# Optimization experiments

Hardware: AMD Instinct MI355X
Metric: run time of the kernel (lower is better)

## Reference

```python
import jax, jax.numpy as jnp
import numpy as np

EMBED = 256
HEADS = 8
HDIM = EMBED // HEADS
TGT = 32400      # bs*H*W = 1*180*180 BEV queries
KLEN = 16896     # bs*num_cams*h*w = 1*6*32*88 image-feature keys
EPS = 1e-5
NEG = -1e9


def _mlp(x, w1, b1, w2, b2):
    # Linear(d,2d) -> ReLU -> Linear(2d,d), torch Linear math with [in,out] weights
    return jax.nn.relu(x @ w1 + b1) @ w2 + b2


def setup_inputs() -> dict:
    rng = np.random.default_rng(0)
    lengths = rng.integers(8, 41, size=KLEN)          # ragged interval sizes
    starts = np.concatenate([[0], np.cumsum(lengths)[:-1]]).astype(np.int32)
    N = int(lengths.sum())
    ranks_feat = np.repeat(np.arange(KLEN, dtype=np.int32), lengths)
    ranks_bev = rng.integers(0, TGT, size=N).astype(np.int32)
    ref_num = int(lengths.max())

    key = jax.random.key(0)
    ks = jax.random.split(key, 16)
    def lin(k, fan_in, fan_out):
        return jax.random.normal(k, (fan_in, fan_out), jnp.float32) / np.sqrt(fan_in)
    return {
        "query": jax.random.normal(ks[0], (TGT, EMBED), jnp.float32),
        "key_in": jax.random.normal(ks[1], (KLEN, EMBED), jnp.float32),
        "value": jax.random.normal(ks[2], (KLEN, EMBED), jnp.float32),
        "ranks_feat": jnp.asarray(ranks_feat),
        "ranks_bev": jnp.asarray(ranks_bev),
        "interval_starts": jnp.asarray(starts),
        "interval_lengths": jnp.asarray(lengths.astype(np.int32)),
        "wq1": lin(ks[3], EMBED, 2 * EMBED), "bq1": jnp.zeros((2 * EMBED,), jnp.float32),
        "wq2": lin(ks[4], 2 * EMBED, EMBED), "bq2": jnp.zeros((EMBED,), jnp.float32),
        "wk1": lin(ks[5], EMBED, 2 * EMBED), "bk1": jnp.zeros((2 * EMBED,), jnp.float32),
        "wk2": lin(ks[6], 2 * EMBED, EMBED), "bk2": jnp.zeros((EMBED,), jnp.float32),
        "ln_g": jnp.ones((EMBED,), jnp.float32), "ln_b": jnp.zeros((EMBED,), jnp.float32),
        "ref_num": ref_num,
    }


def reference(query, key_in, value, ranks_feat, ranks_bev, interval_starts,
              interval_lengths, wq1, bq1, wq2, bq2, wk1, bk1, wk2, bk2,
              ln_g, ln_b, ref_num):
    # interval_lengths only fixes ref_num (static); padding handled via NEG fill.
    N = ranks_feat.shape[0]
    scaling = float(HDIM) ** -0.5

    q = _mlp(query, wq1, bq1, wq2, bq2) * scaling          # [TGT, D]
    k = _mlp(key_in, wk1, bk1, wk2, bk2)                   # [KLEN, D]
    q = q.reshape(TGT, HEADS, HDIM)
    k = k.reshape(KLEN, HEADS, HDIM)
    v = value.reshape(KLEN, HEADS, HDIM)

    # slot index j of each point inside its interval (depth position)
    idx = jnp.arange(N, dtype=jnp.int32)
    seg = jnp.searchsorted(interval_starts, idx, side='right') - 1
    j = idx - interval_starts[seg]

    # per-point q.k logits: q gathered by BEV cell, k by image-feature pixel
    logits = jnp.einsum('nhd,nhd->nh', q[ranks_bev], k[ranks_feat])  # [N,H]

    # dense ragged weight tensor [KLEN, HEADS, ref_num], pad = -1e9
    W = jnp.full((KLEN, HEADS, ref_num), NEG, jnp.float32)
    W = W.at[ranks_feat, :, j].set(logits)
    W_sm = jax.nn.softmax(W, axis=-1)                      # softmax over depth slots

    # gather softmaxed weight per point, weight value, scatter-add to BEV cell
    wp = W_sm[ranks_feat, :, j]                            # [N,H]
    contrib = wp[:, :, None] * v[ranks_feat]               # [N,H,HDIM]
    out = jax.ops.segment_sum(contrib, ranks_bev, num_segments=TGT)
    out = out.reshape(TGT, EMBED)

    # dropout is identity in eval; LayerNorm over embed dim
    mu = jnp.mean(out, axis=-1, keepdims=True)
    var = jnp.mean(jnp.square(out - mu), axis=-1, keepdims=True)
    out = (out - mu) * jax.lax.rsqrt(var + EPS) * ln_g + ln_b
    return out, W_sm
```

## Files before the change

### kernel.cpp

```cpp
#include <hip/hip_runtime.h>
#include <math.h>

#define TGT 32400
#define KLEN 16896
#define EMBED 256
#define HID 512
#define HEADS 8
#define LN_EPS 1e-5f

#define NQT 1013
#define NKT 528
#define HROWS ((NQT + NKT) * 32)

typedef __attribute__((ext_vector_type(8))) short bf16x8;
typedef __attribute__((ext_vector_type(4))) short bf16x4;
typedef __attribute__((ext_vector_type(4))) float f32x4;

__device__ inline short f2bf(float f) {
    union { float f; unsigned u; } v; v.f = f;
    unsigned r = v.u + 0x7FFF + ((v.u >> 16) & 1);
    return (short)(r >> 16);
}
__device__ inline float bf2f(short s) {
    union { unsigned u; float f; } v;
    v.u = ((unsigned)(unsigned short)s) << 16;
    return v.f;
}
__device__ inline void gload_lds16(const short* g, short* l) {
    __builtin_amdgcn_global_load_lds(
        (const __attribute__((address_space(1))) void*)g,
        (__attribute__((address_space(3))) void*)l,
        16, 0, 0);
}

__device__ inline float wave_sum(float v) {
#pragma unroll
    for (int o = 32; o; o >>= 1) v += __shfl_xor(v, o);
    return v;
}
__device__ inline int wave_incl_scan(int v) {
    int lane = threadIdx.x & 63;
#pragma unroll
    for (int o = 1; o < 64; o <<= 1) {
        int x = __shfl_up(v, o);
        if (lane >= o) v += x;
    }
    return v;
}

__global__ __launch_bounds__(256) void prep_kernel(
    const float* __restrict__ value, short* __restrict__ v8,
    const float* __restrict__ wq1, const float* __restrict__ wq2,
    const float* __restrict__ wk1, const float* __restrict__ wk2,
    short* __restrict__ Wt,
    const int* __restrict__ rbev, int N, int* __restrict__ count)
{
    int bid = blockIdx.x;
    if (bid < 2112) {
        int idx = bid * 256 + threadIdx.x;
        int f = idx >> 5;
        int ch = idx & 31;
        const float4* s4 = (const float4*)(value + (size_t)f * 256 + ch * 8);
        float4 a = s4[0], b = s4[1];
        bf16x8 pk;
        pk[0] = f2bf(a.x); pk[1] = f2bf(a.y); pk[2] = f2bf(a.z); pk[3] = f2bf(a.w);
        pk[4] = f2bf(b.x); pk[5] = f2bf(b.y); pk[6] = f2bf(b.z); pk[7] = f2bf(b.w);
        int head = ch >> 2;
        int within = (ch & 3) * 8;
        *(bf16x8*)(v8 + ((size_t)head * KLEN + f) * 32 + within) = pk;
    } else if (bid < 4160) {
        int i = (bid - 2112) * 256 + threadIdx.x;
        int m = i >> 17;
        int r17 = i & 131071;
        int logC = (m & 1) ? 8 : 9;
        int C = 1 << logC;
        int c = r17 & (C - 1);
        int r = r17 >> logC;
        int R = 131072 >> logC;
        const float* W = (m == 0) ? wq1 : (m == 1) ? wq2 : (m == 2) ? wk1 : wk2;
        Wt[(size_t)m * 131072 + (size_t)c * R + r] = f2bf(W[r17]);
    } else {
        int n = (bid - 4160) * 256 + threadIdx.x;
        if (n < N) atomicAdd(&count[rbev[n]], 1);
    }
}

#define XPAD 264
__global__ __launch_bounds__(512, 2) void mlpA_kernel(
    const float* __restrict__ Xq, const float* __restrict__ Xk,
    const short* __restrict__ Wt,
    const float* __restrict__ bq1, const float* __restrict__ bk1,
    short* __restrict__ Hg, int nQblocks)
{
    __shared__ short sX[2][32 * XPAD];

    const int t = threadIdx.x;
    const int wid = t >> 6, lane = t & 63;
    const int lrow = lane & 15, kch = lane >> 4;

    const bool isQ = (int)blockIdx.x < nQblocks;
    const int bid = isQ ? blockIdx.x : blockIdx.x - nQblocks;
    const int stride = isQ ? nQblocks : (gridDim.x - nQblocks);
    const int nT = isQ ? NQT : NKT;
    const int M = isQ ? TGT : KLEN;
    const float* X = isQ ? Xq : Xk;
    const short* W1t = Wt + (size_t)(isQ ? 0 : 2) * 131072;
    const float* b1 = isQ ? bq1 : bk1;
    const int hbase = isQ ? 0 : NQT * 32;

    const int colBase = 64 * wid + lrow;

    bf16x8 w1r[8][4];
#pragma unroll
    for (int ks = 0; ks < 8; ++ks)
#pragma unroll
        for (int j = 0; j < 4; ++j)
            w1r[ks][j] = *(const bf16x8*)(W1t + (size_t)(colBase + 16 * j) * 256 + 32 * ks + 8 * kch);
    float4 bb[4];
#pragma unroll
    for (int j = 0; j < 4; ++j)
        bb[j] = *(const float4*)(b1 + 64 * wid + 16 * j + 4 * kch);

    const int srow = t >> 4, sp = t & 15;

    float4 r0[4], r1[4];
    int tile = bid;
    if (tile < nT) {
        int gr = tile * 32 + srow; if (gr > M - 1) gr = M - 1;
        const float* base = X + (size_t)gr * 256;
#pragma unroll
        for (int i = 0; i < 4; ++i) r0[i] = *(const float4*)(base + (sp + 16 * i) * 4);
    }
    int sel = 0;

    for (; tile < nT; tile += stride) {
#pragma unroll
        for (int i = 0; i < 4; ++i) {
            int c = sp + 16 * i;
            bf16x4 pk;
            pk[0] = f2bf(r0[i].x); pk[1] = f2bf(r0[i].y);
            pk[2] = f2bf(r0[i].z); pk[3] = f2bf(r0[i].w);
            *(bf16x4*)&sX[sel][srow * XPAD + c * 4] = pk;
        }
        int nx = tile + stride;
        if (nx < nT) {
            int gr = nx * 32 + srow; if (gr > M - 1) gr = M - 1;
            const float* base = X + (size_t)gr * 256;
#pragma unroll
            for (int i = 0; i < 4; ++i) r1[i] = *(const float4*)(base + (sp + 16 * i) * 4);
        }
        asm volatile("s_waitcnt lgkmcnt(0)" ::: "memory");
        __builtin_amdgcn_sched_barrier(0);
        __builtin_amdgcn_s_barrier();
        asm volatile("" ::: "memory");

        f32x4 acc[2][4];
#pragma unroll
        for (int rt = 0; rt < 2; ++rt)
#pragma unroll
            for (int j = 0; j < 4; ++j) acc[rt][j] = (f32x4){0.f, 0.f, 0.f, 0.f};

        const short* xs = sX[sel];
#pragma unroll
        for (int ks = 0; ks < 8; ++ks) {
            bf16x8 af[2];
#pragma unroll
            for (int rt = 0; rt < 2; ++rt)
                af[rt] = *(const bf16x8*)&xs[(16 * rt + lrow) * XPAD + 32 * ks + 8 * kch];
#pragma unroll
            for (int j = 0; j < 4; ++j)
#pragma unroll
                for (int rt = 0; rt < 2; ++rt)
                    acc[rt][j] = __builtin_amdgcn_mfma_f32_16x16x32_bf16(w1r[ks][j], af[rt], acc[rt][j], 0, 0, 0);
        }

        int hr0 = hbase + tile * 32;
#pragma unroll
        for (int j = 0; j < 4; ++j) {
#pragma unroll
            for (int rt = 0; rt < 2; ++rt) {
                bf16x4 pk;
                pk[0] = f2bf(fmaxf(acc[rt][j][0] + bb[j].x, 0.f));
                pk[1] = f2bf(fmaxf(acc[rt][j][1] + bb[j].y, 0.f));
                pk[2] = f2bf(fmaxf(acc[rt][j][2] + bb[j].z, 0.f));
                pk[3] = f2bf(fmaxf(acc[rt][j][3] + bb[j].w, 0.f));
                *(bf16x4*)(Hg + (size_t)(hr0 + 16 * rt + lrow) * 512 + 64 * wid + 16 * j + 4 * kch) = pk;
            }
        }
#pragma unroll
        for (int i = 0; i < 4; ++i) r0[i] = r1[i];
        sel ^= 1;
    }
}

__global__ __launch_bounds__(512, 2) void mlpB_kernel(
    const short* __restrict__ Hg, const short* __restrict__ Wt,
    const float* __restrict__ bq2, const float* __restrict__ bk2,
    short* __restrict__ q8, short* __restrict__ k8,
    float scaleQ, int nQblocks)
{
    __shared__ short sX[2][32 * 512];

    const int t = threadIdx.x;
    const int wid = t >> 6, lane = t & 63;
    const int lrow = lane & 15, kch = lane >> 4;

    const bool isQ = (int)blockIdx.x < nQblocks;
    const int bid = isQ ? blockIdx.x : blockIdx.x - nQblocks;
    const int stride = isQ ? nQblocks : (gridDim.x - nQblocks);
    const int nT = isQ ? NQT : NKT;
    const int M = isQ ? TGT : KLEN;
    const short* W2t = Wt + (size_t)(isQ ? 1 : 3) * 131072;
    const float* b2 = isQ ? bq2 : bk2;
    short* Y8 = isQ ? q8 : k8;
    const int hbase = isQ ? 0 : NQT * 32;
    const float scale = isQ ? scaleQ : 1.0f;

    const int colBase = 32 * wid + lrow;

    bf16x8 w2r[16][2];
#pragma unroll
    for (int ks = 0; ks < 16; ++ks)
#pragma unroll
        for (int ct = 0; ct < 2; ++ct)
            w2r[ks][ct] = *(const bf16x8*)(W2t + (size_t)(colBase + 16 * ct) * 512 + 32 * ks + 8 * kch);
    float4 bb[2];
#pragma unroll
    for (int ct = 0; ct < 2; ++ct)
        bb[ct] = *(const float4*)(b2 + 32 * wid + 16 * ct + 4 * kch);

    auto stage = [&](int tt, int s) {
#pragma unroll
        for (int i = 0; i < 4; ++i) {
            int baseslot = i * 512 + wid * 64;
            int slot = baseslot + lane;
            int r = slot >> 6;
            int d = slot & 63;
            int cs = d ^ (r & 7);
            gload_lds16(Hg + (size_t)(hbase + tt * 32 + r) * 512 + cs * 8,
                        &sX[s][baseslot * 8]);
        }
    };

    int tile = bid;
    int sel = 0;
    if (tile < nT) stage(tile, 0);

    for (; tile < nT; tile += stride) {
        asm volatile("s_waitcnt vmcnt(0)" ::: "memory");
        __builtin_amdgcn_sched_barrier(0);
        __builtin_amdgcn_s_barrier();
        asm volatile("" ::: "memory");
        int nx = tile + stride;
        if (nx < nT) stage(nx, sel ^ 1);
        __builtin_amdgcn_sched_barrier(0);

        f32x4 acc[2][2];
#pragma unroll
        for (int ct = 0; ct < 2; ++ct)
#pragma unroll
            for (int rt = 0; rt < 2; ++rt) acc[ct][rt] = (f32x4){0.f, 0.f, 0.f, 0.f};

        const short* xs = sX[sel];
#pragma unroll
        for (int ks = 0; ks < 16; ++ks) {
            bf16x8 hf[2];
#pragma unroll
            for (int rt = 0; rt < 2; ++rt) {
                int row = 16 * rt + lrow;
                hf[rt] = *(const bf16x8*)&xs[row * 512 + (((4 * ks + kch) ^ (row & 7)) << 3)];
            }
#pragma unroll
            for (int ct = 0; ct < 2; ++ct)
#pragma unroll
                for (int rt = 0; rt < 2; ++rt)
                    acc[ct][rt] = __builtin_amdgcn_mfma_f32_16x16x32_bf16(w2r[ks][ct], hf[rt], acc[ct][rt], 0, 0, 0);
        }

        int gr0 = tile * 32;
#pragma unroll
        for (int ct = 0; ct < 2; ++ct) {
#pragma unroll
            for (int rt = 0; rt < 2; ++rt) {
                int gr = gr0 + 16 * rt + lrow;
                if (gr < M) {
                    bf16x4 pk;
                    pk[0] = f2bf((acc[ct][rt][0] + bb[ct].x) * scale);
                    pk[1] = f2bf((acc[ct][rt][1] + bb[ct].y) * scale);
                    pk[2] = f2bf((acc[ct][rt][2] + bb[ct].z) * scale);
                    pk[3] = f2bf((acc[ct][rt][3] + bb[ct].w) * scale);
                    *(bf16x4*)(Y8 + ((size_t)wid * M + gr) * 32 + 16 * ct + 4 * kch) = pk;
                }
            }
        }
        sel ^= 1;
    }
}

__global__ __launch_bounds__(256) void logits8_kernel(
    const short* __restrict__ q8, const short* __restrict__ k8,
    const int* __restrict__ rbev, const int* __restrict__ starts,
    const int* __restrict__ lengths, int rn,
    float* __restrict__ Wsm, short* __restrict__ Wg8)
{
    const int h = blockIdx.x & 7;
    const int fb = blockIdx.x >> 3;
    const int t = threadIdx.x;
    const int w = t >> 6;
    const int lane = t & 63;
    const int fsub = lane >> 3;
    const int js = lane & 7;
    const int f = fb * 32 + w * 8 + fsub;
    const int st = starts[f], len = lengths[f];

    const short* krow = k8 + ((size_t)h * KLEN + f) * 32;
    float kf[32];
#pragma unroll
    for (int cc = 0; cc < 4; ++cc) {
        bf16x8 kv = *(const bf16x8*)(krow + cc * 8);
#pragma unroll
        for (int e = 0; e < 8; ++e) kf[cc * 8 + e] = bf2f(kv[e]);
    }
    const short* qbase = q8 + (size_t)h * TGT * 32;

    float lg[5];
#pragma unroll
    for (int tt = 0; tt < 5; ++tt) {
        int j = js + 8 * tt;
        float s = -3.0e38f;
        if (j < len) {
            int b = rbev[st + j];
            const short* qrow = qbase + (size_t)b * 32;
            s = 0.f;
#pragma unroll
            for (int cc = 0; cc < 4; ++cc) {
                bf16x8 qv = *(const bf16x8*)(qrow + cc * 8);
#pragma unroll
                for (int e = 0; e < 8; ++e) s += bf2f(qv[e]) * kf[cc * 8 + e];
            }
        }
        lg[tt] = s;
    }

    float m = fmaxf(fmaxf(fmaxf(lg[0], lg[1]), fmaxf(lg[2], lg[3])), lg[4]);
    m = fmaxf(m, __shfl_xor(m, 1));
    m = fmaxf(m, __shfl_xor(m, 2));
    m = fmaxf(m, __shfl_xor(m, 4));
    float ex[5];
    float sum = 0.f;
#pragma unroll
    for (int tt = 0; tt < 5; ++tt) {
        int j = js + 8 * tt;
        float e = (j < len) ? __expf(lg[tt] - m) : 0.f;
        ex[tt] = e;
        sum += e;
    }
    sum += __shfl_xor(sum, 1);
    sum += __shfl_xor(sum, 2);
    sum += __shfl_xor(sum, 4);
    float inv = 1.f / sum;

    float* wrow = Wsm + ((size_t)f * HEADS + h) * rn;
    short* grow = Wg8 + ((size_t)h * KLEN + f) * rn;
#pragma unroll
    for (int tt = 0; tt < 5; ++tt) {
        int j = js + 8 * tt;
        if (j < rn) {
            float wv = (j < len) ? ex[tt] * inv : 0.f;
            wrow[j] = wv;
            if (j < len) grow[j] = f2bf(wv);
        }
    }
}

__global__ __launch_bounds__(1024) void scan_kernel(
    const int* __restrict__ count, int n,
    int* __restrict__ offs, int* __restrict__ cursor)
{
    __shared__ int wsum[16];
    __shared__ int carry_s;
    const int t = threadIdx.x;
    const int lane = t & 63, wid = t >> 6;
    if (t == 0) carry_s = 0;
    __syncthreads();

    for (int base = 0; base < n; base += 8192) {
        int idx0 = base + t * 8;
        int v[8];
        if (idx0 + 8 <= n) {
            int4 a = *(const int4*)(count + idx0);
            int4 b = *(const int4*)(count + idx0 + 4);
            v[0] = a.x; v[1] = a.y; v[2] = a.z; v[3] = a.w;
            v[4] = b.x; v[5] = b.y; v[6] = b.z; v[7] = b.w;
        } else {
#pragma unroll
            for (int i = 0; i < 8; ++i) v[i] = (idx0 + i < n) ? count[idx0 + i] : 0;
        }
        int loc[8];
        int s = 0;
#pragma unroll
        for (int i = 0; i < 8; ++i) { loc[i] = s; s += v[i]; }
        int incl = wave_incl_scan(s);
        if (lane == 63) wsum[wid] = incl;
        __syncthreads();
        if (wid == 0) {
            int x = (lane < 16) ? wsum[lane] : 0;
            int xi = wave_incl_scan(x);
            if (lane < 16) wsum[lane] = xi;
        }
        __syncthreads();
        int waveoff = (wid > 0) ? wsum[wid - 1] : 0;
        int carry = carry_s;
        int excl = carry + waveoff + incl - s;
        int o[8];
#pragma unroll
        for (int i = 0; i < 8; ++i) o[i] = excl + loc[i];
        if (idx0 + 8 <= n) {
            *(int4*)(offs + idx0)     = make_int4(o[0], o[1], o[2], o[3]);
            *(int4*)(offs + idx0 + 4) = make_int4(o[4], o[5], o[6], o[7]);
            *(int4*)(cursor + idx0)     = make_int4(o[0], o[1], o[2], o[3]);
            *(int4*)(cursor + idx0 + 4) = make_int4(o[4], o[5], o[6], o[7]);
        } else {
#pragma unroll
            for (int i = 0; i < 8; ++i)
                if (idx0 + i < n) { offs[idx0 + i] = o[i]; cursor[idx0 + i] = o[i]; }
        }
        __syncthreads();
        if (t == 1023) carry_s = carry + waveoff + incl;
        __syncthreads();
    }
    if (t == 0) offs[n] = carry_s;
}

__global__ __launch_bounds__(256) void perm_kernel(
    const int* __restrict__ rbev, const int* __restrict__ rfeat,
    const int* __restrict__ starts, int N,
    int* __restrict__ cursor, int* __restrict__ perm)
{
    int n = blockIdx.x * 256 + threadIdx.x;
    if (n < N) {
        int b = rbev[n];
        int f = rfeat[n];
        int j = n - starts[f];
        int pos = atomicAdd(&cursor[b], 1);
        perm[pos] = (f << 6) | j;
    }
}

__global__ __launch_bounds__(256) void gather8_kernel(
    const short* __restrict__ v8, const short* __restrict__ Wg8,
    const int* __restrict__ perm, const int* __restrict__ offs, int rn,
    float* __restrict__ out)
{
    const int h = blockIdx.x & 7;
    const int rb = blockIdx.x >> 3;
    const int t = threadIdx.x;
    const int r = rb * 32 + (t >> 3);
    if (r >= TGT) return;
    const int c = t & 7;
    const int lane = t & 63;
    const int gl = lane & ~7;
    const short* vbase = v8 + (size_t)h * KLEN * 32 + c * 4;
    const short* wbase = Wg8 + (size_t)h * KLEN * rn;
    const int beg = offs[r], end = offs[r + 1];
    const int cnt = end - beg;
    float4 acc = make_float4(0.f, 0.f, 0.f, 0.f);

    for (int base = 0; base < cnt; base += 8) {
        int pk = 0;
        if (base + c < cnt) pk = perm[beg + base + c];
#pragma unroll
        for (int u = 0; u < 8; ++u) {
            int pku = __shfl(pk, gl + u);
            bool valid = (base + u < cnt);
            int fo = pku >> 6, j = pku & 63;
            float w = valid ? bf2f(wbase[(size_t)fo * rn + j]) : 0.f;
            bf16x4 vv = *(const bf16x4*)(vbase + (size_t)fo * 32);
            acc.x += w * bf2f(vv[0]);
            acc.y += w * bf2f(vv[1]);
            acc.z += w * bf2f(vv[2]);
            acc.w += w * bf2f(vv[3]);
        }
    }
    *(float4*)(out + (size_t)r * EMBED + h * 32 + c * 4) = acc;
}

__global__ __launch_bounds__(256) void ln_kernel(
    float* __restrict__ out, const float* __restrict__ g, const float* __restrict__ b)
{
    int row = blockIdx.x * 4 + (threadIdx.x >> 6);
    if (row >= TGT) return;
    int lane = threadIdx.x & 63;
    float4 x = *(float4*)(out + (size_t)row * EMBED + lane * 4);
    float mu = wave_sum(x.x + x.y + x.z + x.w) * (1.f / EMBED);
    float dx = x.x - mu, dy = x.y - mu, dz = x.z - mu, dw = x.w - mu;
    float var = wave_sum(dx * dx + dy * dy + dz * dz + dw * dw) * (1.f / EMBED);
    float rs = rsqrtf(var + LN_EPS);
    float4 gg = *(const float4*)(g + lane * 4);
    float4 bb = *(const float4*)(b + lane * 4);
    float4 y;
    y.x = dx * rs * gg.x + bb.x;
    y.y = dy * rs * gg.y + bb.y;
    y.z = dz * rs * gg.z + bb.z;
    y.w = dw * rs * gg.w + bb.w;
    *(float4*)(out + (size_t)row * EMBED + lane * 4) = y;
}

extern "C" void kernel_launch(void* const* d_in, const int* in_sizes, int n_in,
                              void* d_out, int out_size, void* d_ws, size_t ws_size,
                              hipStream_t stream) {
    const float* query  = (const float*)d_in[0];
    const float* key_in = (const float*)d_in[1];
    const float* value  = (const float*)d_in[2];
    const int* rfeat    = (const int*)d_in[3];
    const int* rbev     = (const int*)d_in[4];
    const int* starts   = (const int*)d_in[5];
    const int* lengths  = (const int*)d_in[6];
    const float* wq1 = (const float*)d_in[7];
    const float* bq1 = (const float*)d_in[8];
    const float* wq2 = (const float*)d_in[9];
    const float* bq2 = (const float*)d_in[10];
    const float* wk1 = (const float*)d_in[11];
    const float* bk1 = (const float*)d_in[12];
    const float* wk2 = (const float*)d_in[13];
    const float* bk2 = (const float*)d_in[14];
    const float* ln_g = (const float*)d_in[15];
    const float* ln_b = (const float*)d_in[16];

    const int N = in_sizes[3];
    const int rn = (out_size - TGT * EMBED) / (KLEN * HEADS);

    float* outp = (float*)d_out;
    float* Wsm  = outp + (size_t)TGT * EMBED;

    short* Hg   = (short*)d_ws;
    short* q8   = Hg + (size_t)HROWS * 512;
    short* k8   = q8 + (size_t)TGT * EMBED;
    short* v8   = k8 + (size_t)KLEN * EMBED;
    short* Wt   = v8 + (size_t)KLEN * EMBED;
    short* Wg8  = Wt + 4 * 131072;
    int* count  = (int*)(Wg8 + (size_t)HEADS * KLEN * rn);
    int* offs   = count + TGT;
    int* cursor = offs + TGT + 1;
    int* perm   = cursor + TGT;

    const float scaling = 0.1767766952966369f;
    const int nQblocks = 168;

    hipMemsetAsync(count, 0, TGT * sizeof(int), stream);

    int hist_blocks = (N + 255) / 256;
    prep_kernel<<<4160 + hist_blocks, 256, 0, stream>>>(
        value, v8, wq1, wq2, wk1, wk2, Wt, rbev, N, count);

    mlpA_kernel<<<256, 512, 0, stream>>>(query, key_in, Wt, bq1, bk1, Hg, nQblocks);
    mlpB_kernel<<<256, 512, 0, stream>>>(Hg, Wt, bq2, bk2, q8, k8, scaling, nQblocks);

    scan_kernel<<<1, 1024, 0, stream>>>(count, TGT, offs, cursor);
    perm_kernel<<<(N + 255) / 256, 256, 0, stream>>>(rbev, rfeat, starts, N, cursor, perm);

    logits8_kernel<<<8 * (KLEN / 32), 256, 0, stream>>>(
        q8, k8, rbev, starts, lengths, rn, Wsm, Wg8);

    gather8_kernel<<<8 * ((TGT + 31) / 32), 256, 0, stream>>>(
        v8, Wg8, perm, offs, rn, outp);
    ln_kernel<<<(TGT + 3) / 4, 256, 0, stream>>>(outp, ln_g, ln_b);
}
```

Before: 207.6 us.

## Sort BEV rows by point count to balance gather work across waves

Adds a count histogram in the scan kernel and a new rowsort kernel that builds a row permutation grouping rows with similar point counts. The gather kernel processes rows in this permuted order, which reduces intra-wave divergence from uneven segment lengths. The gather loop is also unrolled to 16 points per iteration, to get more memory loads in flight. In exchange there is an extra launch, shared-memory atomics in the single-block scan, and scattered output row writes.

```diff
diff --git a/kernel.cpp b/kernel.cpp
--- a/kernel.cpp
+++ b/kernel.cpp
@@ -375,13 +375,17 @@
 
 __global__ __launch_bounds__(1024) void scan_kernel(
     const int* __restrict__ count, int n,
-    int* __restrict__ offs, int* __restrict__ cursor)
+    int* __restrict__ offs, int* __restrict__ cursor,
+    int* __restrict__ cursor64)
 {
     __shared__ int wsum[16];
+    __shared__ int hist[4][64];
     __shared__ int carry_s;
     const int t = threadIdx.x;
     const int lane = t & 63, wid = t >> 6;
+    const int rep = t >> 8;
     if (t == 0) carry_s = 0;
+    if (t < 256) hist[t >> 6][t & 63] = 0;
     __syncthreads();
 
     for (int base = 0; base < n; base += 8192) {
@@ -396,6 +400,13 @@
 #pragma unroll
             for (int i = 0; i < 8; ++i) v[i] = (idx0 + i < n) ? count[idx0 + i] : 0;
         }
+#pragma unroll
+        for (int i = 0; i < 8; ++i) {
+            if (idx0 + i < n) {
+                int c = v[i]; if (c > 63) c = 63;
+                atomicAdd(&hist[rep][c], 1);
+            }
+        }
         int loc[8];
         int s = 0;
 #pragma unroll
@@ -429,7 +440,35 @@
         if (t == 1023) carry_s = carry + waveoff + incl;
         __syncthreads();
     }
+    if (t < 64) {
+        int tot = hist[0][t] + hist[1][t] + hist[2][t] + hist[3][t];
+        int incl = wave_incl_scan(tot);
+        cursor64[t] = incl - tot;
+    }
     if (t == 0) offs[n] = carry_s;
+}
+
+__global__ __launch_bounds__(256) void rowsort_kernel(
+    const int* __restrict__ offs, int* __restrict__ cursor64,
+    int* __restrict__ rowperm)
+{
+    __shared__ int lh[64];
+    __shared__ int lbase[64];
+    const int t = threadIdx.x;
+    if (t < 64) lh[t] = 0;
+    __syncthreads();
+    int r = blockIdx.x * 256 + t;
+    int cnt = 0, lpos = 0;
+    bool ok = r < TGT;
+    if (ok) {
+        cnt = offs[r + 1] - offs[r];
+        if (cnt > 63) cnt = 63;
+        lpos = atomicAdd(&lh[cnt], 1);
+    }
+    __syncthreads();
+    if (t < 64 && lh[t] > 0) lbase[t] = atomicAdd(&cursor64[t], lh[t]);
+    __syncthreads();
+    if (ok) rowperm[lbase[cnt] + lpos] = r;
 }
 
 __global__ __launch_bounds__(256) void perm_kernel(
@@ -449,14 +488,16 @@
 
 __global__ __launch_bounds__(256) void gather8_kernel(
     const short* __restrict__ v8, const short* __restrict__ Wg8,
-    const int* __restrict__ perm, const int* __restrict__ offs, int rn,
+    const int* __restrict__ perm, const int* __restrict__ offs,
+    const int* __restrict__ rowperm, int rn,
     float* __restrict__ out)
 {
     const int h = blockIdx.x & 7;
     const int rb = blockIdx.x >> 3;
     const int t = threadIdx.x;
-    const int r = rb * 32 + (t >> 3);
-    if (r >= TGT) return;
+    const int idx = rb * 32 + (t >> 3);
+    if (idx >= TGT) return;
+    const int r = rowperm[idx];
     const int c = t & 7;
     const int lane = t & 63;
     const int gl = lane & ~7;
@@ -466,12 +507,12 @@
     const int cnt = end - beg;
     float4 acc = make_float4(0.f, 0.f, 0.f, 0.f);
 
-    for (int base = 0; base < cnt; base += 8) {
-        int pk = 0;
-        if (base + c < cnt) pk = perm[beg + base + c];
-#pragma unroll
-        for (int u = 0; u < 8; ++u) {
-            int pku = __shfl(pk, gl + u);
+    for (int base = 0; base < cnt; base += 16) {
+        int pk0 = (base + c < cnt) ? perm[beg + base + c] : 0;
+        int pk1 = (base + 8 + c < cnt) ? perm[beg + base + 8 + c] : 0;
+#pragma unroll
+        for (int u = 0; u < 16; ++u) {
+            int pku = __shfl(u < 8 ? pk0 : pk1, gl + (u & 7));
             bool valid = (base + u < cnt);
             int fo = pku >> 6, j = pku & 63;
             float w = valid ? bf2f(wbase[(size_t)fo * rn + j]) : 0.f;
@@ -543,6 +584,8 @@
     int* offs   = count + TGT;
     int* cursor = offs + TGT + 1;
     int* perm   = cursor + TGT;
+    int* rowperm = perm + N;
+    int* cursor64 = rowperm + TGT;
 
     const float scaling = 0.1767766952966369f;
     const int nQblocks = 168;
@@ -556,13 +599,14 @@
     mlpA_kernel<<<256, 512, 0, stream>>>(query, key_in, Wt, bq1, bk1, Hg, nQblocks);
     mlpB_kernel<<<256, 512, 0, stream>>>(Hg, Wt, bq2, bk2, q8, k8, scaling, nQblocks);
 
-    scan_kernel<<<1, 1024, 0, stream>>>(count, TGT, offs, cursor);
+    scan_kernel<<<1, 1024, 0, stream>>>(count, TGT, offs, cursor, cursor64);
+    rowsort_kernel<<<(TGT + 255) / 256, 256, 0, stream>>>(offs, cursor64, rowperm);
     perm_kernel<<<(N + 255) / 256, 256, 0, stream>>>(rbev, rfeat, starts, N, cursor, perm);
 
     logits8_kernel<<<8 * (KLEN / 32), 256, 0, stream>>>(
         q8, k8, rbev, starts, lengths, rn, Wsm, Wg8);
 
     gather8_kernel<<<8 * ((TGT + 31) / 32), 256, 0, stream>>>(
-        v8, Wg8, perm, offs, rn, outp);
+        v8, Wg8, perm, offs, rowperm, rn, outp);
     ln_kernel<<<(TGT + 3) / 4, 256, 0, stream>>>(outp, ln_g, ln_b);
 }
```

Result: slower. 218.0 us (+5.0%).
